# Kernel tuning notes

Measured on AMD Instinct MI355X. Metric: run time of the kernel, lower is better.

## Reference

```python
import jax, jax.numpy as jnp
import numpy as np

D_MODEL = 1024
NUM_HEAD = 16
HEAD_DIM = D_MODEL // NUM_HEAD  # 64


def setup_inputs() -> dict:
    key = jax.random.key(0)
    ks = jax.random.split(key, 9)
    B, S = 2, 2048
    s = 0.02
    return {
        "x": jax.random.normal(ks[0], (B, S, D_MODEL), dtype=jnp.float32),
        "Wq": jax.random.normal(ks[1], (D_MODEL, D_MODEL), dtype=jnp.float32) * s,
        "bq": jax.random.normal(ks[2], (D_MODEL,), dtype=jnp.float32) * s,
        "Wk": jax.random.normal(ks[3], (D_MODEL, D_MODEL), dtype=jnp.float32) * s,
        "bk": jax.random.normal(ks[4], (D_MODEL,), dtype=jnp.float32) * s,
        "Wv": jax.random.normal(ks[5], (D_MODEL, D_MODEL), dtype=jnp.float32) * s,
        "bv": jax.random.normal(ks[6], (D_MODEL,), dtype=jnp.float32) * s,
        "Wo": jax.random.normal(ks[7], (D_MODEL, D_MODEL), dtype=jnp.float32) * s,
        "bo": jax.random.normal(ks[8], (D_MODEL,), dtype=jnp.float32) * s,
    }


def _split_head(t):
    # [B,S,D] -> [B,H,S,hd]
    B, S, _ = t.shape
    return t.reshape(B, S, NUM_HEAD, HEAD_DIM).transpose(0, 2, 1, 3)


def reference(x, Wq, bq, Wk, bk, Wv, bv, Wo, bo):
    B, S, D = x.shape
    q = _split_head(x @ Wq.T + bq)  # [B,H,S,hd]
    k = _split_head(x @ Wk.T + bk)
    v = _split_head(x @ Wv.T + bv)
    scale = 1.0 / jnp.sqrt(jnp.asarray(HEAD_DIM, dtype=x.dtype))
    scores = jnp.einsum("bhqd,bhkd->bhqk", q, k) * scale  # [B,H,S,S]
    attn = jax.nn.softmax(scores, axis=-1)
    out = jnp.einsum("bhqk,bhkd->bhqd", attn, v)  # [B,H,S,hd]
    out = out.transpose(0, 2, 1, 3).reshape(B, S, D)
    return out @ Wo.T + bo
```

## Files before the change

### kernel.cpp

```cpp
#include <hip/hip_runtime.h>
#include <cstdint>


typedef unsigned short ush;
typedef __bf16 bf16x8 __attribute__((ext_vector_type(8)));
typedef float f32x4 __attribute__((ext_vector_type(4)));
typedef ush u16x8 __attribute__((ext_vector_type(8)));
typedef ush u16x4 __attribute__((ext_vector_type(4)));

__device__ __forceinline__ ush f2bf(float f) {
  unsigned int u = __float_as_uint(f);
  u += 0x7fffu + ((u >> 16) & 1u);
  return (ush)(u >> 16);
}

__device__ __forceinline__ unsigned int pack2bf_ru(float a, float b) {
  unsigned int ua = __float_as_uint(a) + 0x8000u;
  unsigned int ub = __float_as_uint(b) + 0x8000u;
  return __builtin_amdgcn_perm(ub, ua, 0x07060302u);
}

__device__ __forceinline__ bf16x8 bc8(u16x8 v) {
  return __builtin_bit_cast(bf16x8, v);
}

__device__ __forceinline__ void async16(const void* g, void* l) {
  __builtin_amdgcn_global_load_lds(
      (const __attribute__((address_space(1))) unsigned int*)(uintptr_t)g,
      (__attribute__((address_space(3))) unsigned int*)(uintptr_t)l, 16, 0, 0);
}

__global__ __launch_bounds__(256) void convert_kernel(
    const float* __restrict__ x, const float* __restrict__ Wq,
    const float* __restrict__ Wk, const float* __restrict__ Wv,
    const float* __restrict__ Wo,
    ush* __restrict__ xb, ush* __restrict__ Wqb, ush* __restrict__ Wkb,
    ush* __restrict__ Wvb, ush* __restrict__ Wob)
{
  int tid = blockIdx.x * 256 + threadIdx.x;
  int base = tid * 4;
  const float* src; ush* dst; int idx;
  if (base < 4194304) { src = x; dst = xb; idx = base; }
  else {
    int r = base - 4194304;
    int seg = r >> 20;
    idx = r & 1048575;
    src = seg == 0 ? Wq : seg == 1 ? Wk : seg == 2 ? Wv : Wo;
    dst = seg == 0 ? Wqb : seg == 1 ? Wkb : seg == 2 ? Wvb : Wob;
  }
  float4 f = *(const float4*)(src + idx);
  u16x4 u = { f2bf(f.x), f2bf(f.y), f2bf(f.z), f2bf(f.w) };
  *(u16x4*)(dst + idx) = u;
}

__device__ __forceinline__ void gemm128_core(
    const ush* __restrict__ gA, const ush* __restrict__ gB,
    int m0, int n0, ush* lA, ush* lB, f32x4 (&acc)[4][4])
{
  const int t = threadIdx.x, w = t >> 6, lane = t & 63;
  const int l15 = lane & 15, quad = lane >> 4;
  const int wm = (w >> 1) * 64, wn = (w & 1) * 64;
#pragma unroll
  for (int i = 0; i < 4; ++i)
#pragma unroll
    for (int j = 0; j < 4; ++j) acc[i][j] = (f32x4){0.f, 0.f, 0.f, 0.f};

  for (int kt = 0; kt < 1024; kt += 64) {
#pragma unroll
    for (int i = 0; i < 4; ++i) {
      int j = i * 256 + w * 64 + lane;
      int row = j >> 3, cc = (j & 7) ^ (row & 7);
      async16(gA + (size_t)(m0 + row) * 1024 + kt + cc * 8,
              lA + (i * 256 + w * 64) * 8);
    }
#pragma unroll
    for (int i = 0; i < 4; ++i) {
      int j = i * 256 + w * 64 + lane;
      int row = j >> 3, cc = (j & 7) ^ (row & 7);
      async16(gB + (size_t)(n0 + row) * 1024 + kt + cc * 8,
              lB + (i * 256 + w * 64) * 8);
    }
    __syncthreads();
#pragma unroll
    for (int kf = 0; kf < 2; ++kf) {
      bf16x8 aF[4], bF[4];
#pragma unroll
      for (int mt = 0; mt < 4; ++mt) {
        int row = wm + mt * 16 + l15;
        aF[mt] = bc8(*(const u16x8*)(lA + row * 64 + (((kf * 4 + quad) ^ (row & 7)) * 8)));
      }
#pragma unroll
      for (int nt = 0; nt < 4; ++nt) {
        int row = wn + nt * 16 + l15;
        bF[nt] = bc8(*(const u16x8*)(lB + row * 64 + (((kf * 4 + quad) ^ (row & 7)) * 8)));
      }
#pragma unroll
      for (int mt = 0; mt < 4; ++mt)
#pragma unroll
        for (int nt = 0; nt < 4; ++nt)
          acc[mt][nt] = __builtin_amdgcn_mfma_f32_16x16x32_bf16(
              aF[mt], bF[nt], acc[mt][nt], 0, 0, 0);
    }
    __syncthreads();
  }
}

__global__ __launch_bounds__(256, 2) void qkv_gemm(
    const ush* __restrict__ xb, const ush* __restrict__ Wqb,
    const ush* __restrict__ Wkb, const ush* __restrict__ Wvb,
    const float* __restrict__ bq, const float* __restrict__ bk,
    const float* __restrict__ bv,
    ush* __restrict__ q, ush* __restrict__ k, ush* __restrict__ vt)
{
  int bid = blockIdx.x;
  int wsel = bid >> 8;
  int rem = bid & 255;
  int m0 = (rem & 31) * 128;
  int n0 = (rem >> 5) * 128;
  const ush* gB = wsel == 0 ? Wqb : wsel == 1 ? Wkb : Wvb;
  const float* bias = wsel == 0 ? bq : wsel == 1 ? bk : bv;
  const float oscale = wsel == 1 ? 0.180336880f : 1.0f;

  __shared__ alignas(16) ush lA[128 * 64];
  __shared__ alignas(16) ush lB[128 * 64];
  f32x4 acc[4][4];
  gemm128_core(xb, gB, m0, n0, lA, lB, acc);

  const int t = threadIdx.x, w = t >> 6, lane = t & 63;
  const int l15 = lane & 15, quad = lane >> 4;
  const int wm = (w >> 1) * 64, wn = (w & 1) * 64;
  if (wsel == 2) {
#pragma unroll
    for (int nt = 0; nt < 4; ++nt) {
      int o = n0 + wn + nt * 16 + l15;
      float bl = bias[o];
      int h = o >> 6, d = o & 63;
#pragma unroll
      for (int mt = 0; mt < 4; ++mt) {
        int tb = m0 + wm + mt * 16 + quad * 4;
        int b = tb >> 11, s = tb & 2047;
        u16x4 pk = { f2bf(acc[mt][nt][0] + bl), f2bf(acc[mt][nt][1] + bl),
                     f2bf(acc[mt][nt][2] + bl), f2bf(acc[mt][nt][3] + bl) };
        *(u16x4*)(vt + (size_t)(((b * 16 + h) * 64) + d) * 2048 + s) = pk;
      }
    }
  } else {
    ush* dst = wsel == 0 ? q : k;
#pragma unroll
    for (int nt = 0; nt < 4; ++nt) {
      int o = n0 + wn + nt * 16 + l15;
      float bl = bias[o];
      int h = o >> 6, d = o & 63;
#pragma unroll
      for (int mt = 0; mt < 4; ++mt)
#pragma unroll
        for (int r = 0; r < 4; ++r) {
          int token = m0 + wm + mt * 16 + quad * 4 + r;
          int b = token >> 11, s = token & 2047;
          dst[(size_t)(((b * 16 + h) * 2048) + s) * 64 + d] =
              f2bf((acc[mt][nt][r] + bl) * oscale);
        }
    }
  }
}

__global__ __launch_bounds__(256, 4) void attn_kernel(
    const ush* __restrict__ Q, const ush* __restrict__ K,
    const ush* __restrict__ VT, ush* __restrict__ O)
{
  const int bid = blockIdx.x;
  const int bh = (bid & 7) * 4 + (bid >> 8);
  const int qt = (bid >> 3) & 31;
  const ush* qb = Q + (size_t)bh * 2048 * 64;
  const ush* kb = K + (size_t)bh * 2048 * 64;
  const ush* vtb = VT + (size_t)bh * 64 * 2048;
  const int t = threadIdx.x, w = t >> 6, lane = t & 63;
  const int l15 = lane & 15, quad = lane >> 4;
  const int q0 = qt * 64 + w * 16;

  __shared__ alignas(16) ush lK[2][64 * 64];
  __shared__ alignas(16) ush lV[2][64 * 64];
  __shared__ alignas(16) ush lP[4][16 * 64];

  const int r0 = t >> 3;
  const int c0 = (t & 7) ^ (r0 & 7);
  const ush* kSrc0 = kb + (size_t)r0 * 64 + c0 * 8;
  const ush* kSrc1 = kb + (size_t)(r0 + 32) * 64 + c0 * 8;
  const ush* vSrc0 = vtb + (size_t)r0 * 2048 + c0 * 8;
  const ush* vSrc1 = vtb + (size_t)(r0 + 32) * 2048 + c0 * 8;

  bf16x8 qF[2];
#pragma unroll
  for (int kf = 0; kf < 2; ++kf)
    qF[kf] = bc8(*(const u16x8*)(qb + (size_t)(q0 + l15) * 64 + kf * 32 + quad * 8));

  float li = 0.f;
  f32x4 accO[4];
#pragma unroll
  for (int dt = 0; dt < 4; ++dt) accO[dt] = (f32x4){0.f, 0.f, 0.f, 0.f};

  async16(kSrc0, lK[0] + t * 8);
  async16(kSrc1, lK[0] + (t + 256) * 8);
  async16(vSrc0, lV[0] + t * 8);
  async16(vSrc1, lV[0] + (t + 256) * 8);
  __syncthreads();

  for (int it = 0; it < 32; ++it) {
    const int cur = it & 1, nxt = cur ^ 1;
    if (it + 1 < 32) {
      const size_t ko = (size_t)(it + 1) * 64 * 64;
      const int vo = (it + 1) * 64;
      async16(kSrc0 + ko, lK[nxt] + t * 8);
      async16(kSrc1 + ko, lK[nxt] + (t + 256) * 8);
      async16(vSrc0 + vo, lV[nxt] + t * 8);
      async16(vSrc1 + vo, lV[nxt] + (t + 256) * 8);
    }
    const ush* lk = lK[cur];
    const ush* lv = lV[cur];

    f32x4 sc[4];
#pragma unroll
    for (int mt = 0; mt < 4; ++mt) sc[mt] = (f32x4){0.f, 0.f, 0.f, 0.f};
#pragma unroll
    for (int kf = 0; kf < 2; ++kf) {
#pragma unroll
      for (int mt = 0; mt < 4; ++mt) {
        int row = mt * 16 + l15;
        bf16x8 aK = bc8(*(const u16x8*)(lk + row * 64 + (((kf * 4 + quad) ^ (row & 7)) * 8)));
        sc[mt] = __builtin_amdgcn_mfma_f32_16x16x32_bf16(aK, qF[kf], sc[mt], 0, 0, 0);
      }
    }

    float rs = 0.f;
#pragma unroll
    for (int mt = 0; mt < 4; ++mt) {
      f32x4 p;
#pragma unroll
      for (int r = 0; r < 4; ++r) {
        p[r] = __builtin_amdgcn_exp2f(sc[mt][r]);
        rs += p[r];
      }
      uint2 pw = { pack2bf_ru(p[0], p[1]), pack2bf_ru(p[2], p[3]) };
      int chunk = mt * 2 + (quad >> 1);
      *(uint2*)(&lP[w][l15 * 64 + ((chunk ^ (l15 & 7)) * 8) + (quad & 1) * 4]) = pw;
    }
    rs += __shfl_xor(rs, 16);
    rs += __shfl_xor(rs, 32);
    li += rs;

    __builtin_amdgcn_wave_barrier();

    bf16x8 aP[2];
#pragma unroll
    for (int kf = 0; kf < 2; ++kf)
      aP[kf] = bc8(*(const u16x8*)(&lP[w][l15 * 64 + (((kf * 4 + quad) ^ (l15 & 7)) * 8)]));
#pragma unroll
    for (int kf = 0; kf < 2; ++kf) {
#pragma unroll
      for (int dt = 0; dt < 4; ++dt) {
        int row = dt * 16 + l15;
        bf16x8 bV = bc8(*(const u16x8*)(lv + row * 64 + (((kf * 4 + quad) ^ (row & 7)) * 8)));
        accO[dt] = __builtin_amdgcn_mfma_f32_16x16x32_bf16(aP[kf], bV, accO[dt], 0, 0, 0);
      }
    }
    __syncthreads();
  }

  const int b = bh >> 4, h = bh & 15;
  float linv[4];
#pragma unroll
  for (int r = 0; r < 4; ++r)
    linv[r] = __builtin_amdgcn_rcpf(__shfl(li, quad * 4 + r));
#pragma unroll
  for (int dt = 0; dt < 4; ++dt)
#pragma unroll
    for (int r = 0; r < 4; ++r) {
      int s = q0 + quad * 4 + r;
      O[(size_t)(b * 2048 + s) * 1024 + h * 64 + dt * 16 + l15] =
          f2bf(accO[dt][r] * linv[r]);
    }
}

__global__ __launch_bounds__(256, 2) void out_gemm(
    const ush* __restrict__ ab, const ush* __restrict__ Wob,
    const float* __restrict__ bo, float* __restrict__ out)
{
  int rem = blockIdx.x;
  int m0 = (rem & 31) * 128;
  int n0 = (rem >> 5) * 128;
  __shared__ alignas(16) ush lA[128 * 64];
  __shared__ alignas(16) ush lB[128 * 64];
  f32x4 acc[4][4];
  gemm128_core(ab, Wob, m0, n0, lA, lB, acc);

  const int t = threadIdx.x, w = t >> 6, lane = t & 63;
  const int l15 = lane & 15, quad = lane >> 4;
  const int wm = (w >> 1) * 64, wn = (w & 1) * 64;
#pragma unroll
  for (int nt = 0; nt < 4; ++nt) {
    int o = n0 + wn + nt * 16 + l15;
    float bl = bo[o];
#pragma unroll
    for (int mt = 0; mt < 4; ++mt)
#pragma unroll
      for (int r = 0; r < 4; ++r) {
        int token = m0 + wm + mt * 16 + quad * 4 + r;
        out[(size_t)token * 1024 + o] = acc[mt][nt][r] + bl;
      }
  }
}

extern "C" void kernel_launch(void* const* d_in, const int* in_sizes, int n_in,
                              void* d_out, int out_size, void* d_ws, size_t ws_size,
                              hipStream_t stream)
{
  const float* x  = (const float*)d_in[0];
  const float* Wq = (const float*)d_in[1];
  const float* bq = (const float*)d_in[2];
  const float* Wk = (const float*)d_in[3];
  const float* bk = (const float*)d_in[4];
  const float* Wv = (const float*)d_in[5];
  const float* bv = (const float*)d_in[6];
  const float* Wo = (const float*)d_in[7];
  const float* bo = (const float*)d_in[8];
  float* out = (float*)d_out;

  char* ws = (char*)d_ws;
  ush* xb  = (ush*)(ws);
  ush* Wqb = (ush*)(ws + (size_t)( 8u << 20));
  ush* Wkb = (ush*)(ws + (size_t)(10u << 20));
  ush* Wvb = (ush*)(ws + (size_t)(12u << 20));
  ush* Wob = (ush*)(ws + (size_t)(14u << 20));
  ush* qb  = (ush*)(ws + (size_t)(16u << 20));
  ush* kb  = (ush*)(ws + (size_t)(24u << 20));
  ush* vtb = (ush*)(ws + (size_t)(32u << 20));
  ush* ab  = (ush*)(ws + (size_t)(40u << 20));

  convert_kernel<<<8192, 256, 0, stream>>>(x, Wq, Wk, Wv, Wo,
                                           xb, Wqb, Wkb, Wvb, Wob);
  qkv_gemm<<<768, 256, 0, stream>>>(xb, Wqb, Wkb, Wvb, bq, bk, bv, qb, kb, vtb);
  attn_kernel<<<1024, 256, 0, stream>>>(qb, kb, vtb, ab);
  out_gemm<<<256, 256, 0, stream>>>(ab, Wob, bo, out);
}
```

Measured before the change: 188.2 us.

## Keep attention probabilities in registers and halve out-GEMM N tile

```diff
diff --git a/kernel.cpp b/kernel.cpp
--- a/kernel.cpp
+++ b/kernel.cpp
@@ -7,6 +7,7 @@
 typedef float f32x4 __attribute__((ext_vector_type(4)));
 typedef ush u16x8 __attribute__((ext_vector_type(8)));
 typedef ush u16x4 __attribute__((ext_vector_type(4)));
+typedef unsigned int u32x4 __attribute__((ext_vector_type(4)));
 
 __device__ __forceinline__ ush f2bf(float f) {
   unsigned int u = __float_as_uint(f);
@@ -180,7 +181,6 @@
 
   __shared__ alignas(16) ush lK[2][64 * 64];
   __shared__ alignas(16) ush lV[2][64 * 64];
-  __shared__ alignas(16) ush lP[4][16 * 64];
 
   const int r0 = t >> 3;
   const int c0 = (t & 7) ^ (r0 & 7);
@@ -198,6 +198,10 @@
   f32x4 accO[4];
 #pragma unroll
   for (int dt = 0; dt < 4; ++dt) accO[dt] = (f32x4){0.f, 0.f, 0.f, 0.f};
+
+  const int sw = l15 & 7;
+  const int qh = (quad & 1) * 4;
+  const int qg = quad >> 1;
 
   async16(kSrc0, lK[0] + t * 8);
   async16(kSrc1, lK[0] + (t + 256) * 8);
@@ -232,53 +236,48 @@
     }
 
     float rs = 0.f;
-#pragma unroll
-    for (int mt = 0; mt < 4; ++mt) {
-      f32x4 p;
+    f32x4 p[4];
+#pragma unroll
+    for (int mt = 0; mt < 4; ++mt)
 #pragma unroll
       for (int r = 0; r < 4; ++r) {
-        p[r] = __builtin_amdgcn_exp2f(sc[mt][r]);
-        rs += p[r];
-      }
-      uint2 pw = { pack2bf_ru(p[0], p[1]), pack2bf_ru(p[2], p[3]) };
-      int chunk = mt * 2 + (quad >> 1);
-      *(uint2*)(&lP[w][l15 * 64 + ((chunk ^ (l15 & 7)) * 8) + (quad & 1) * 4]) = pw;
-    }
+        p[mt][r] = __builtin_amdgcn_exp2f(sc[mt][r]);
+        rs += p[mt][r];
+      }
     rs += __shfl_xor(rs, 16);
     rs += __shfl_xor(rs, 32);
     li += rs;
 
-    __builtin_amdgcn_wave_barrier();
-
-    bf16x8 aP[2];
-#pragma unroll
-    for (int kf = 0; kf < 2; ++kf)
-      aP[kf] = bc8(*(const u16x8*)(&lP[w][l15 * 64 + (((kf * 4 + quad) ^ (l15 & 7)) * 8)]));
-#pragma unroll
-    for (int kf = 0; kf < 2; ++kf) {
+#pragma unroll
+    for (int ks = 0; ks < 2; ++ks) {
+      u32x4 bw = { pack2bf_ru(p[2 * ks][0],     p[2 * ks][1]),
+                   pack2bf_ru(p[2 * ks][2],     p[2 * ks][3]),
+                   pack2bf_ru(p[2 * ks + 1][0], p[2 * ks + 1][1]),
+                   pack2bf_ru(p[2 * ks + 1][2], p[2 * ks + 1][3]) };
+      bf16x8 bP = __builtin_bit_cast(bf16x8, bw);
+      int c1 = ((ks * 4 + qg) ^ sw) * 8 + qh;
+      int c2 = ((ks * 4 + 2 + qg) ^ sw) * 8 + qh;
 #pragma unroll
       for (int dt = 0; dt < 4; ++dt) {
-        int row = dt * 16 + l15;
-        bf16x8 bV = bc8(*(const u16x8*)(lv + row * 64 + (((kf * 4 + quad) ^ (row & 7)) * 8)));
-        accO[dt] = __builtin_amdgcn_mfma_f32_16x16x32_bf16(aP[kf], bV, accO[dt], 0, 0, 0);
+        const ush* base = lv + (dt * 16 + l15) * 64;
+        u16x4 a0 = *(const u16x4*)(base + c1);
+        u16x4 a1 = *(const u16x4*)(base + c2);
+        u16x8 av = { a0[0], a0[1], a0[2], a0[3], a1[0], a1[1], a1[2], a1[3] };
+        accO[dt] = __builtin_amdgcn_mfma_f32_16x16x32_bf16(bc8(av), bP, accO[dt], 0, 0, 0);
       }
     }
     __syncthreads();
   }
 
   const int b = bh >> 4, h = bh & 15;
-  float linv[4];
-#pragma unroll
-  for (int r = 0; r < 4; ++r)
-    linv[r] = __builtin_amdgcn_rcpf(__shfl(li, quad * 4 + r));
-#pragma unroll
-  for (int dt = 0; dt < 4; ++dt)
-#pragma unroll
-    for (int r = 0; r < 4; ++r) {
-      int s = q0 + quad * 4 + r;
-      O[(size_t)(b * 2048 + s) * 1024 + h * 64 + dt * 16 + l15] =
-          f2bf(accO[dt][r] * linv[r]);
-    }
+  const float linv = __builtin_amdgcn_rcpf(li);
+  const int s = q0 + l15;
+#pragma unroll
+  for (int dt = 0; dt < 4; ++dt) {
+    u16x4 pk = { f2bf(accO[dt][0] * linv), f2bf(accO[dt][1] * linv),
+                 f2bf(accO[dt][2] * linv), f2bf(accO[dt][3] * linv) };
+    *(u16x4*)(O + (size_t)(b * 2048 + s) * 1024 + h * 64 + dt * 16 + quad * 4) = pk;
+  }
 }
 
 __global__ __launch_bounds__(256, 2) void out_gemm(
@@ -287,17 +286,58 @@
 {
   int rem = blockIdx.x;
   int m0 = (rem & 31) * 128;
-  int n0 = (rem >> 5) * 128;
+  int n0 = (rem >> 5) * 64;
   __shared__ alignas(16) ush lA[128 * 64];
-  __shared__ alignas(16) ush lB[128 * 64];
-  f32x4 acc[4][4];
-  gemm128_core(ab, Wob, m0, n0, lA, lB, acc);
+  __shared__ alignas(16) ush lB[64 * 64];
 
   const int t = threadIdx.x, w = t >> 6, lane = t & 63;
   const int l15 = lane & 15, quad = lane >> 4;
-  const int wm = (w >> 1) * 64, wn = (w & 1) * 64;
-#pragma unroll
-  for (int nt = 0; nt < 4; ++nt) {
+  const int wm = (w >> 1) * 64, wn = (w & 1) * 32;
+  f32x4 acc[4][2];
+#pragma unroll
+  for (int i = 0; i < 4; ++i)
+#pragma unroll
+    for (int j = 0; j < 2; ++j) acc[i][j] = (f32x4){0.f, 0.f, 0.f, 0.f};
+
+  for (int kt = 0; kt < 1024; kt += 64) {
+#pragma unroll
+    for (int i = 0; i < 4; ++i) {
+      int j = i * 256 + t;
+      int row = j >> 3, cc = (j & 7) ^ (row & 7);
+      async16(ab + (size_t)(m0 + row) * 1024 + kt + cc * 8, lA + j * 8);
+    }
+#pragma unroll
+    for (int i = 0; i < 2; ++i) {
+      int j = i * 256 + t;
+      int row = j >> 3, cc = (j & 7) ^ (row & 7);
+      async16(Wob + (size_t)(n0 + row) * 1024 + kt + cc * 8, lB + j * 8);
+    }
+    __syncthreads();
+#pragma unroll
+    for (int kf = 0; kf < 2; ++kf) {
+      bf16x8 aF[4], bF[2];
+#pragma unroll
+      for (int mt = 0; mt < 4; ++mt) {
+        int row = wm + mt * 16 + l15;
+        aF[mt] = bc8(*(const u16x8*)(lA + row * 64 + (((kf * 4 + quad) ^ (row & 7)) * 8)));
+      }
+#pragma unroll
+      for (int nt = 0; nt < 2; ++nt) {
+        int row = wn + nt * 16 + l15;
+        bF[nt] = bc8(*(const u16x8*)(lB + row * 64 + (((kf * 4 + quad) ^ (row & 7)) * 8)));
+      }
+#pragma unroll
+      for (int mt = 0; mt < 4; ++mt)
+#pragma unroll
+        for (int nt = 0; nt < 2; ++nt)
+          acc[mt][nt] = __builtin_amdgcn_mfma_f32_16x16x32_bf16(
+              aF[mt], bF[nt], acc[mt][nt], 0, 0, 0);
+    }
+    __syncthreads();
+  }
+
+#pragma unroll
+  for (int nt = 0; nt < 2; ++nt) {
     int o = n0 + wn + nt * 16 + l15;
     float bl = bo[o];
 #pragma unroll
@@ -340,5 +380,5 @@
                                            xb, Wqb, Wkb, Wvb, Wob);
   qkv_gemm<<<768, 256, 0, stream>>>(xb, Wqb, Wkb, Wvb, bq, bk, bv, qb, kb, vtb);
   attn_kernel<<<1024, 256, 0, stream>>>(qb, kb, vtb, ab);
-  out_gemm<<<256, 256, 0, stream>>>(ab, Wob, bo, out);
-}
+  out_gemm<<<512, 256, 0, stream>>>(ab, Wob, bo, out);
+}
```

Measured after the change: 198.6 us. 1.06x slower.

## Keep P in registers via permuted V^T layout and 2 q-groups per wave

Applied to the files above, without the earlier changes.

```diff
diff --git a/kernel.cpp b/kernel.cpp
--- a/kernel.cpp
+++ b/kernel.cpp
@@ -7,6 +7,7 @@
 typedef float f32x4 __attribute__((ext_vector_type(4)));
 typedef ush u16x8 __attribute__((ext_vector_type(8)));
 typedef ush u16x4 __attribute__((ext_vector_type(4)));
+typedef unsigned int u32x4 __attribute__((ext_vector_type(4)));
 
 __device__ __forceinline__ ush f2bf(float f) {
   unsigned int u = __float_as_uint(f);
@@ -139,9 +140,11 @@
       for (int mt = 0; mt < 4; ++mt) {
         int tb = m0 + wm + mt * 16 + quad * 4;
         int b = tb >> 11, s = tb & 2047;
+        int so = s & 63;
+        int sp = (s & ~63) | (so & 35) | ((so & 12) << 1) | ((so & 16) >> 2);
         u16x4 pk = { f2bf(acc[mt][nt][0] + bl), f2bf(acc[mt][nt][1] + bl),
                      f2bf(acc[mt][nt][2] + bl), f2bf(acc[mt][nt][3] + bl) };
-        *(u16x4*)(vt + (size_t)(((b * 16 + h) * 64) + d) * 2048 + s) = pk;
+        *(u16x4*)(vt + (size_t)(((b * 16 + h) * 64) + d) * 2048 + sp) = pk;
       }
     }
   } else {
@@ -164,7 +167,7 @@
   }
 }
 
-__global__ __launch_bounds__(256, 4) void attn_kernel(
+__global__ __launch_bounds__(128, 2) void attn_kernel(
     const ush* __restrict__ Q, const ush* __restrict__ K,
     const ush* __restrict__ VT, ush* __restrict__ O)
 {
@@ -176,33 +179,36 @@
   const ush* vtb = VT + (size_t)bh * 64 * 2048;
   const int t = threadIdx.x, w = t >> 6, lane = t & 63;
   const int l15 = lane & 15, quad = lane >> 4;
-  const int q0 = qt * 64 + w * 16;
+  const int q0 = qt * 64 + w * 32;
 
   __shared__ alignas(16) ush lK[2][64 * 64];
   __shared__ alignas(16) ush lV[2][64 * 64];
-  __shared__ alignas(16) ush lP[4][16 * 64];
 
   const int r0 = t >> 3;
   const int c0 = (t & 7) ^ (r0 & 7);
-  const ush* kSrc0 = kb + (size_t)r0 * 64 + c0 * 8;
-  const ush* kSrc1 = kb + (size_t)(r0 + 32) * 64 + c0 * 8;
-  const ush* vSrc0 = vtb + (size_t)r0 * 2048 + c0 * 8;
-  const ush* vSrc1 = vtb + (size_t)(r0 + 32) * 2048 + c0 * 8;
-
-  bf16x8 qF[2];
-#pragma unroll
-  for (int kf = 0; kf < 2; ++kf)
-    qF[kf] = bc8(*(const u16x8*)(qb + (size_t)(q0 + l15) * 64 + kf * 32 + quad * 8));
-
-  float li = 0.f;
-  f32x4 accO[4];
-#pragma unroll
-  for (int dt = 0; dt < 4; ++dt) accO[dt] = (f32x4){0.f, 0.f, 0.f, 0.f};
-
-  async16(kSrc0, lK[0] + t * 8);
-  async16(kSrc1, lK[0] + (t + 256) * 8);
-  async16(vSrc0, lV[0] + t * 8);
-  async16(vSrc1, lV[0] + (t + 256) * 8);
+  const ush* kSrc = kb + (size_t)r0 * 64 + c0 * 8;
+  const ush* vSrc = vtb + (size_t)r0 * 2048 + c0 * 8;
+
+  bf16x8 qF[2][2];
+#pragma unroll
+  for (int g = 0; g < 2; ++g)
+#pragma unroll
+    for (int kf = 0; kf < 2; ++kf)
+      qF[g][kf] = bc8(*(const u16x8*)(qb + (size_t)(q0 + g * 16 + l15) * 64 +
+                                      kf * 32 + quad * 8));
+
+  float li[2] = {0.f, 0.f};
+  f32x4 accO[2][4];
+#pragma unroll
+  for (int g = 0; g < 2; ++g)
+#pragma unroll
+    for (int dt = 0; dt < 4; ++dt) accO[g][dt] = (f32x4){0.f, 0.f, 0.f, 0.f};
+
+#pragma unroll
+  for (int i = 0; i < 4; ++i) {
+    async16(kSrc + i * 1024, lK[0] + (i * 128 + t) * 8);
+    async16(vSrc + (size_t)i * 16 * 2048, lV[0] + (i * 128 + t) * 8);
+  }
   __syncthreads();
 
   for (int it = 0; it < 32; ++it) {
@@ -210,75 +216,83 @@
     if (it + 1 < 32) {
       const size_t ko = (size_t)(it + 1) * 64 * 64;
       const int vo = (it + 1) * 64;
-      async16(kSrc0 + ko, lK[nxt] + t * 8);
-      async16(kSrc1 + ko, lK[nxt] + (t + 256) * 8);
-      async16(vSrc0 + vo, lV[nxt] + t * 8);
-      async16(vSrc1 + vo, lV[nxt] + (t + 256) * 8);
+#pragma unroll
+      for (int i = 0; i < 4; ++i) {
+        async16(kSrc + ko + i * 1024, lK[nxt] + (i * 128 + t) * 8);
+        async16(vSrc + vo + (size_t)i * 16 * 2048, lV[nxt] + (i * 128 + t) * 8);
+      }
     }
     const ush* lk = lK[cur];
     const ush* lv = lV[cur];
 
-    f32x4 sc[4];
-#pragma unroll
-    for (int mt = 0; mt < 4; ++mt) sc[mt] = (f32x4){0.f, 0.f, 0.f, 0.f};
+    f32x4 sc[2][4];
+#pragma unroll
+    for (int g = 0; g < 2; ++g)
+#pragma unroll
+      for (int mt = 0; mt < 4; ++mt) sc[g][mt] = (f32x4){0.f, 0.f, 0.f, 0.f};
 #pragma unroll
     for (int kf = 0; kf < 2; ++kf) {
 #pragma unroll
       for (int mt = 0; mt < 4; ++mt) {
         int row = mt * 16 + l15;
         bf16x8 aK = bc8(*(const u16x8*)(lk + row * 64 + (((kf * 4 + quad) ^ (row & 7)) * 8)));
-        sc[mt] = __builtin_amdgcn_mfma_f32_16x16x32_bf16(aK, qF[kf], sc[mt], 0, 0, 0);
-      }
-    }
-
-    float rs = 0.f;
-#pragma unroll
-    for (int mt = 0; mt < 4; ++mt) {
-      f32x4 p;
-#pragma unroll
-      for (int r = 0; r < 4; ++r) {
-        p[r] = __builtin_amdgcn_exp2f(sc[mt][r]);
-        rs += p[r];
-      }
-      uint2 pw = { pack2bf_ru(p[0], p[1]), pack2bf_ru(p[2], p[3]) };
-      int chunk = mt * 2 + (quad >> 1);
-      *(uint2*)(&lP[w][l15 * 64 + ((chunk ^ (l15 & 7)) * 8) + (quad & 1) * 4]) = pw;
-    }
-    rs += __shfl_xor(rs, 16);
-    rs += __shfl_xor(rs, 32);
-    li += rs;
-
-    __builtin_amdgcn_wave_barrier();
-
-    bf16x8 aP[2];
-#pragma unroll
-    for (int kf = 0; kf < 2; ++kf)
-      aP[kf] = bc8(*(const u16x8*)(&lP[w][l15 * 64 + (((kf * 4 + quad) ^ (l15 & 7)) * 8)]));
-#pragma unroll
-    for (int kf = 0; kf < 2; ++kf) {
-#pragma unroll
-      for (int dt = 0; dt < 4; ++dt) {
-        int row = dt * 16 + l15;
-        bf16x8 bV = bc8(*(const u16x8*)(lv + row * 64 + (((kf * 4 + quad) ^ (row & 7)) * 8)));
-        accO[dt] = __builtin_amdgcn_mfma_f32_16x16x32_bf16(aP[kf], bV, accO[dt], 0, 0, 0);
+#pragma unroll
+        for (int g = 0; g < 2; ++g)
+          sc[g][mt] = __builtin_amdgcn_mfma_f32_16x16x32_bf16(
+              aK, qF[g][kf], sc[g][mt], 0, 0, 0);
+      }
+    }
+
+    float rs[2] = {0.f, 0.f};
+#pragma unroll
+    for (int g = 0; g < 2; ++g) {
+#pragma unroll
+      for (int mt = 0; mt < 4; ++mt)
+#pragma unroll
+        for (int r = 0; r < 4; ++r) {
+          sc[g][mt][r] = __builtin_amdgcn_exp2f(sc[g][mt][r]);
+          rs[g] += sc[g][mt][r];
+        }
+      rs[g] += __shfl_xor(rs[g], 16);
+      rs[g] += __shfl_xor(rs[g], 32);
+      li[g] += rs[g];
+    }
+
+#pragma unroll
+    for (int ks = 0; ks < 2; ++ks) {
+      bf16x8 aV[4];
+#pragma unroll
+      for (int dt = 0; dt < 4; ++dt)
+        aV[dt] = bc8(*(const u16x8*)(lv + (dt * 16 + l15) * 64 +
+                                     (((ks * 4 + quad) ^ (l15 & 7)) * 8)));
+#pragma unroll
+      for (int g = 0; g < 2; ++g) {
+        u32x4 bw = { pack2bf_ru(sc[g][2 * ks][0],     sc[g][2 * ks][1]),
+                     pack2bf_ru(sc[g][2 * ks][2],     sc[g][2 * ks][3]),
+                     pack2bf_ru(sc[g][2 * ks + 1][0], sc[g][2 * ks + 1][1]),
+                     pack2bf_ru(sc[g][2 * ks + 1][2], sc[g][2 * ks + 1][3]) };
+        bf16x8 bP = __builtin_bit_cast(bf16x8, bw);
+#pragma unroll
+        for (int dt = 0; dt < 4; ++dt)
+          accO[g][dt] = __builtin_amdgcn_mfma_f32_16x16x32_bf16(
+              aV[dt], bP, accO[g][dt], 0, 0, 0);
       }
     }
     __syncthreads();
   }
 
   const int b = bh >> 4, h = bh & 15;
-  float linv[4];
-#pragma unroll
-  for (int r = 0; r < 4; ++r)
-    linv[r] = __builtin_amdgcn_rcpf(__shfl(li, quad * 4 + r));
-#pragma unroll
-  for (int dt = 0; dt < 4; ++dt)
-#pragma unroll
-    for (int r = 0; r < 4; ++r) {
-      int s = q0 + quad * 4 + r;
-      O[(size_t)(b * 2048 + s) * 1024 + h * 64 + dt * 16 + l15] =
-          f2bf(accO[dt][r] * linv[r]);
-    }
+#pragma unroll
+  for (int g = 0; g < 2; ++g) {
+    const float linv = __builtin_amdgcn_rcpf(li[g]);
+    const int s = q0 + g * 16 + l15;
+#pragma unroll
+    for (int dt = 0; dt < 4; ++dt) {
+      u16x4 pk = { f2bf(accO[g][dt][0] * linv), f2bf(accO[g][dt][1] * linv),
+                   f2bf(accO[g][dt][2] * linv), f2bf(accO[g][dt][3] * linv) };
+      *(u16x4*)(O + (size_t)(b * 2048 + s) * 1024 + h * 64 + dt * 16 + quad * 4) = pk;
+    }
+  }
 }
 
 __global__ __launch_bounds__(256, 2) void out_gemm(
@@ -339,6 +353,6 @@
   convert_kernel<<<8192, 256, 0, stream>>>(x, Wq, Wk, Wv, Wo,
                                            xb, Wqb, Wkb, Wvb, Wob);
   qkv_gemm<<<768, 256, 0, stream>>>(xb, Wqb, Wkb, Wvb, bq, bk, bv, qb, kb, vtb);
-  attn_kernel<<<1024, 256, 0, stream>>>(qb, kb, vtb, ab);
+  attn_kernel<<<1024, 128, 0, stream>>>(qb, kb, vtb, ab);
   out_gemm<<<256, 256, 0, stream>>>(ab, Wob, bo, out);
 }
```

New measurement: 186.9 us. Within noise of the previous version (-0.7%).
